# Kernel optimization log

Hardware: AMD Instinct MI355X
Metric: run time of the kernel (lower is better)

Reference implementation:

```python
import math
import jax, jax.numpy as jnp
import numpy as np

N, H, W = 512, 256, 256


def setup_inputs() -> dict:
    key = jax.random.key(0)
    k1, k2, k3 = jax.random.split(key, 3)
    # means uniform over the image plane, as in the torch __init__
    means = jax.random.uniform(k1, (N, 2), jnp.float32) * jnp.array([W, H], jnp.float32)
    # rgbs default 0.5 -> logit 0; perturb slightly for a non-degenerate test point
    rgb_logits = 0.1 * jax.random.normal(k2, (N, 3), jnp.float32)
    opacity_logits = jnp.zeros((N,), jnp.float32)
    # cholesky init: diag = log(expm1(scale)), off-diag 0 (scale = sqrt(H*W/N)*0.5)
    scale = math.sqrt(H * W / N) * 0.5
    diag = math.log(math.expm1(scale))
    cholesky_raw = jnp.stack([
        jnp.full((N,), diag, jnp.float32) + 0.05 * jax.random.normal(k3, (N,), jnp.float32),
        jnp.zeros((N,), jnp.float32),
        jnp.full((N,), diag, jnp.float32),
    ], axis=1)
    return {"means": means, "cholesky_raw": cholesky_raw,
            "rgb_logits": rgb_logits, "opacity_logits": opacity_logits}


def _render(means, cholesky_raw, rgb_logits, opacity_logits):
    # --- project_gaussians_cholesky: Cholesky -> covariance -> conic (inverse cov) ---
    L11 = jax.nn.softplus(cholesky_raw[:, 0])
    L21 = cholesky_raw[:, 1]
    L22 = jax.nn.softplus(cholesky_raw[:, 2])
    s00 = L11 * L11          # Sigma = L L^T
    s01 = L11 * L21
    s11 = L21 * L21 + L22 * L22
    det = (L11 * L22) ** 2   # det(Sigma)
    a = s11 / det            # conic = Sigma^{-1}, packed (a, b, c)
    b = -s01 / det
    c = s00 / det

    rgbs = jax.nn.sigmoid(rgb_logits)          # [N,3]
    opac = jax.nn.sigmoid(opacity_logits)      # [N]

    # --- rasterize: dense per-pixel evaluation, alpha-composited in gaussian order ---
    px = jnp.arange(W, dtype=jnp.float32) + 0.5
    py = jnp.arange(H, dtype=jnp.float32) + 0.5
    dX = means[:, 0, None, None] - px[None, None, :]   # [N,1,W]
    dY = means[:, 1, None, None] - py[None, :, None]   # [N,H,1]
    a3 = a[:, None, None]; b3 = b[:, None, None]; c3 = c[:, None, None]
    sigma = 0.5 * (a3 * dX * dX + c3 * dY * dY) + b3 * dX * dY   # [N,H,W]
    alpha = jnp.minimum(opac[:, None, None] * jnp.exp(-sigma), 0.999)

    # transmittance T_i = prod_{j<i} (1 - alpha_j), via exclusive cumsum in log space
    log1m = jnp.log1p(-alpha)
    logT = jnp.concatenate([jnp.zeros((1, H, W), alpha.dtype),
                            jnp.cumsum(log1m, axis=0)[:-1]], axis=0)
    vis = alpha * jnp.exp(logT)                # [N,H,W] compositing weight

    img = jnp.einsum('nhw,nc->hwc', vis, rgbs)     # [H,W,3]
    wsum = jnp.sum(vis, axis=0)                    # [H,W]

    # upscale gradients: d alpha / d(pixel x,y) per gaussian, composited with T
    gx = a3 * dX + b3 * dY
    gy = b3 * dX + c3 * dY
    dx_img = jnp.einsum('nhw,nc->hwc', vis * gx, rgbs)
    dy_img = jnp.einsum('nhw,nc->hwc', vis * gy, rgbs)
    dxy_img = jnp.einsum('nhw,nc->hwc', vis * (gx * gy - b3), rgbs)
    return img, wsum, dx_img, dy_img, dxy_img


def reference(means, cholesky_raw, rgb_logits, opacity_logits):
    img, wsum, dx_img, dy_img, dxy_img = _render(means, cholesky_raw, rgb_logits, opacity_logits)
    render = jnp.transpose(img, (2, 0, 1))  # CHW
    return (render, img, wsum, dx_img, dy_img, dxy_img)
```

## Files before the change

### kernel.cpp

```cpp
#include <hip/hip_runtime.h>
#include <math.h>

#define NG 512
#define HH 256
#define WW 256
#define TILE 8
#define TXN (WW / TILE)
#define TYN (HH / TILE)
#define NTILES (TXN * TYN)
#define CHUNKS 8
#define NACC 13
#define S_CUT 12.0f

__device__ __forceinline__ float softplus_f(float x) {
    if (x > 20.0f) return x;
    if (x < -20.0f) return expf(x);
    return log1pf(expf(x));
}

__device__ __forceinline__ float sigmoid_f(float x) {
    return 1.0f / (1.0f + expf(-x));
}

__global__ void prep_kernel(const float* __restrict__ means,
                            const float* __restrict__ chol,
                            const float* __restrict__ rgbl,
                            const float* __restrict__ opl,
                            float* __restrict__ params,
                            int4* __restrict__ tb) {
    int n = blockIdx.x * blockDim.x + threadIdx.x;
    if (n >= NG) return;
    float L11 = softplus_f(chol[3*n + 0]);
    float L21 = chol[3*n + 1];
    float L22 = softplus_f(chol[3*n + 2]);
    float s00 = L11 * L11;
    float s01 = L11 * L21;
    float s11 = L21 * L21 + L22 * L22;
    float d  = L11 * L22;
    float inv = 1.0f / (d * d);
    float mx = means[2*n + 0];
    float my = means[2*n + 1];
    float* p = params + 12 * n;
    p[0] = mx;
    p[1] = my;
    p[2] =  s11 * inv;
    p[3] = -s01 * inv;
    p[4] =  s00 * inv;
    p[5] = sigmoid_f(opl[n]);
    p[6] = sigmoid_f(rgbl[3*n + 0]);
    p[7] = sigmoid_f(rgbl[3*n + 1]);
    p[8] = sigmoid_f(rgbl[3*n + 2]);
    p[9] = 0.0f; p[10] = 0.0f; p[11] = 0.0f;

    float ex = sqrtf(2.0f * S_CUT * s00);
    float ey = sqrtf(2.0f * S_CUT * s11);
    int4 r;
    r.x = max(0,       (int)floorf((mx - ex) * (1.0f / TILE)));
    r.y = min(TXN - 1, (int)floorf((mx + ex) * (1.0f / TILE)));
    r.z = max(0,       (int)floorf((my - ey) * (1.0f / TILE)));
    r.w = min(TYN - 1, (int)floorf((my + ey) * (1.0f / TILE)));
    tb[n] = r;
}

__global__ __launch_bounds__(512, 8)
void render_kernel(const float* __restrict__ params,
                   const int4* __restrict__ tb,
                   float* __restrict__ out) {
    const int lane = threadIdx.x & 63;
    const int wv   = threadIdx.x >> 6;
    const int tx   = blockIdx.x & (TXN - 1);
    const int ty   = blockIdx.x >> 5;
    const int x0   = tx * TILE;
    const int y0   = ty * TILE;
    const float px = (float)(x0 + (lane & 7)) + 0.5f;
    const float py = (float)(y0 + (lane >> 3)) + 0.5f;

    int4 bb = tb[threadIdx.x];
    bool hit = (tx >= bb.x) && (tx <= bb.y) && (ty >= bb.z) && (ty <= bb.w);
    unsigned long long m = __ballot(hit ? 1 : 0);

    const float4* __restrict__ g4 = (const float4*)params;
    const int cbase = wv * 64;

    float T = 1.0f;
    float ir = 0.f, ig = 0.f, ib = 0.f, wsum = 0.f;
    float xr = 0.f, xg = 0.f, xb = 0.f;
    float yr = 0.f, yg = 0.f, yb = 0.f;
    float qr = 0.f, qg = 0.f, qb = 0.f;

    while (m) {
        int n = __builtin_ctzll(m);
        m &= (m - 1);
        int gi = __builtin_amdgcn_readfirstlane(cbase + n);
        float4 P0 = g4[3*gi + 0];
        float4 P1 = g4[3*gi + 1];
        float4 P2 = g4[3*gi + 2];
        float dX = P0.x - px;
        float dY = P0.y - py;
        float a = P0.z, b = P0.w, c = P1.x, opac = P1.y;
        float gx = a * dX + b * dY;
        float gy = b * dX + c * dY;
        float s  = 0.5f * (dX * gx + dY * gy);
        float e  = __expf(-s);
        float alpha = fminf(opac * e, 0.999f);
        float vis = alpha * T;
        T = T - alpha * T;
        wsum += vis;
        float r = P1.z, g = P1.w, bcol = P2.x;
        ir += vis * r;  ig += vis * g;  ib += vis * bcol;
        float vgx = vis * gx;
        float vgy = vis * gy;
        xr += vgx * r;  xg += vgx * g;  xb += vgx * bcol;
        yr += vgy * r;  yg += vgy * g;  yb += vgy * bcol;
        float q  = gx * gy - b;
        float vq = vis * q;
        qr += vq * r;   qg += vq * g;   qb += vq * bcol;
    }

    __shared__ float Tl[CHUNKS][64];
    __shared__ float accL[NACC][CHUNKS][64];
    Tl[wv][lane] = T;
    __syncthreads();

    float scale = 1.0f;
    for (int i = 0; i < wv; ++i) scale *= Tl[i][lane];

    accL[ 0][wv][lane] = ir   * scale;
    accL[ 1][wv][lane] = ig   * scale;
    accL[ 2][wv][lane] = ib   * scale;
    accL[ 3][wv][lane] = wsum * scale;
    accL[ 4][wv][lane] = xr   * scale;
    accL[ 5][wv][lane] = xg   * scale;
    accL[ 6][wv][lane] = xb   * scale;
    accL[ 7][wv][lane] = yr   * scale;
    accL[ 8][wv][lane] = yg   * scale;
    accL[ 9][wv][lane] = yb   * scale;
    accL[10][wv][lane] = qr   * scale;
    accL[11][wv][lane] = qg   * scale;
    accL[12][wv][lane] = qb   * scale;
    __syncthreads();

    const int HW = HH * WW;
    for (int v = threadIdx.x; v < 64 * NACC; v += 512) {
        int pp   = v / NACC;
        int comp = v - pp * NACC;
        float s = 0.f;
        #pragma unroll
        for (int cch = 0; cch < CHUNKS; ++cch) s += accL[comp][cch][pp];
        int p = (y0 + (pp >> 3)) * WW + x0 + (pp & 7);
        if (comp < 3) {
            out[comp * HW + p] = s;
            out[3 * HW + 3 * p + comp] = s;
        } else if (comp == 3) {
            out[6 * HW + p] = s;
        } else if (comp < 7) {
            out[7 * HW + 3 * p + (comp - 4)] = s;
        } else if (comp < 10) {
            out[10 * HW + 3 * p + (comp - 7)] = s;
        } else {
            out[13 * HW + 3 * p + (comp - 10)] = s;
        }
    }
}

extern "C" void kernel_launch(void* const* d_in, const int* in_sizes, int n_in,
                              void* d_out, int out_size, void* d_ws, size_t ws_size,
                              hipStream_t stream) {
    const float* means = (const float*)d_in[0];
    const float* chol  = (const float*)d_in[1];
    const float* rgbl  = (const float*)d_in[2];
    const float* opl   = (const float*)d_in[3];
    float* out = (float*)d_out;
    float* params = (float*)d_ws;
    int4*  tb     = (int4*)((char*)d_ws + 24 * 1024);

    prep_kernel<<<dim3(2), dim3(256), 0, stream>>>(means, chol, rgbl, opl, params, tb);
    render_kernel<<<dim3(NTILES), dim3(512), 0, stream>>>(params, tb, out);
}
```

Before: 71.73 us.

## Fuse gaussian preprocessing into render kernel with per-block LDS parameters

Removes the separate prep kernel and has every render block recompute all 512 gaussians' conic, colors, opacity and tile-overlap test itself, storing parameters in shared memory. The per-gaussian parameter reads then come from LDS instead of global memory, and one kernel launch plus the inter-kernel dependency disappear. In exchange every one of the 1024 blocks redoes the softplus, sigmoid and sqrt work for all gaussians. The LDS buffer is reused for the accumulator reduction. The bounding test now uses float comparisons against tile edges instead of integer tile indices.

```diff
diff --git a/kernel.cpp b/kernel.cpp
--- a/kernel.cpp
+++ b/kernel.cpp
@@ -22,52 +22,15 @@
     return 1.0f / (1.0f + expf(-x));
 }
 
-__global__ void prep_kernel(const float* __restrict__ means,
-                            const float* __restrict__ chol,
-                            const float* __restrict__ rgbl,
-                            const float* __restrict__ opl,
-                            float* __restrict__ params,
-                            int4* __restrict__ tb) {
-    int n = blockIdx.x * blockDim.x + threadIdx.x;
-    if (n >= NG) return;
-    float L11 = softplus_f(chol[3*n + 0]);
-    float L21 = chol[3*n + 1];
-    float L22 = softplus_f(chol[3*n + 2]);
-    float s00 = L11 * L11;
-    float s01 = L11 * L21;
-    float s11 = L21 * L21 + L22 * L22;
-    float d  = L11 * L22;
-    float inv = 1.0f / (d * d);
-    float mx = means[2*n + 0];
-    float my = means[2*n + 1];
-    float* p = params + 12 * n;
-    p[0] = mx;
-    p[1] = my;
-    p[2] =  s11 * inv;
-    p[3] = -s01 * inv;
-    p[4] =  s00 * inv;
-    p[5] = sigmoid_f(opl[n]);
-    p[6] = sigmoid_f(rgbl[3*n + 0]);
-    p[7] = sigmoid_f(rgbl[3*n + 1]);
-    p[8] = sigmoid_f(rgbl[3*n + 2]);
-    p[9] = 0.0f; p[10] = 0.0f; p[11] = 0.0f;
-
-    float ex = sqrtf(2.0f * S_CUT * s00);
-    float ey = sqrtf(2.0f * S_CUT * s11);
-    int4 r;
-    r.x = max(0,       (int)floorf((mx - ex) * (1.0f / TILE)));
-    r.y = min(TXN - 1, (int)floorf((mx + ex) * (1.0f / TILE)));
-    r.z = max(0,       (int)floorf((my - ey) * (1.0f / TILE)));
-    r.w = min(TYN - 1, (int)floorf((my + ey) * (1.0f / TILE)));
-    tb[n] = r;
-}
-
 __global__ __launch_bounds__(512, 8)
-void render_kernel(const float* __restrict__ params,
-                   const int4* __restrict__ tb,
+void render_kernel(const float* __restrict__ means,
+                   const float* __restrict__ chol,
+                   const float* __restrict__ rgbl,
+                   const float* __restrict__ opl,
                    float* __restrict__ out) {
-    const int lane = threadIdx.x & 63;
-    const int wv   = threadIdx.x >> 6;
+    const int tid  = threadIdx.x;
+    const int lane = tid & 63;
+    const int wv   = tid >> 6;
     const int tx   = blockIdx.x & (TXN - 1);
     const int ty   = blockIdx.x >> 5;
     const int x0   = tx * TILE;
@@ -75,11 +38,36 @@
     const float px = (float)(x0 + (lane & 7)) + 0.5f;
     const float py = (float)(y0 + (lane >> 3)) + 0.5f;
 
-    int4 bb = tb[threadIdx.x];
-    bool hit = (tx >= bb.x) && (tx <= bb.y) && (ty >= bb.z) && (ty <= bb.w);
+    __shared__ float shbuf[NACC * CHUNKS * 64];
+    __shared__ float Tl[CHUNKS][64];
+
+    bool hit;
+    {
+        float L11 = softplus_f(chol[3*tid + 0]);
+        float L21 = chol[3*tid + 1];
+        float L22 = softplus_f(chol[3*tid + 2]);
+        float s00 = L11 * L11;
+        float s01 = L11 * L21;
+        float s11 = L21 * L21 + L22 * L22;
+        float dd  = L11 * L22;
+        float inv = 1.0f / (dd * dd);
+        float mx  = means[2*tid + 0];
+        float my  = means[2*tid + 1];
+        float4* p4 = (float4*)shbuf;
+        p4[3*tid + 0] = make_float4(mx, my, s11 * inv, -s01 * inv);
+        p4[3*tid + 1] = make_float4(s00 * inv, sigmoid_f(opl[tid]),
+                                    sigmoid_f(rgbl[3*tid + 0]),
+                                    sigmoid_f(rgbl[3*tid + 1]));
+        p4[3*tid + 2] = make_float4(sigmoid_f(rgbl[3*tid + 2]), 0.f, 0.f, 0.f);
+        float ex = sqrtf(2.0f * S_CUT * s00);
+        float ey = sqrtf(2.0f * S_CUT * s11);
+        hit = (mx - ex < (float)(x0 + TILE)) && (mx + ex > (float)x0) &&
+              (my - ey < (float)(y0 + TILE)) && (my + ey > (float)y0);
+    }
     unsigned long long m = __ballot(hit ? 1 : 0);
+    __syncthreads();
 
-    const float4* __restrict__ g4 = (const float4*)params;
+    const float4* __restrict__ g4 = (const float4*)shbuf;
     const int cbase = wv * 64;
 
     float T = 1.0f;
@@ -117,36 +105,38 @@
         qr += vq * r;   qg += vq * g;   qb += vq * bcol;
     }
 
-    __shared__ float Tl[CHUNKS][64];
-    __shared__ float accL[NACC][CHUNKS][64];
     Tl[wv][lane] = T;
     __syncthreads();
 
     float scale = 1.0f;
     for (int i = 0; i < wv; ++i) scale *= Tl[i][lane];
 
-    accL[ 0][wv][lane] = ir   * scale;
-    accL[ 1][wv][lane] = ig   * scale;
-    accL[ 2][wv][lane] = ib   * scale;
-    accL[ 3][wv][lane] = wsum * scale;
-    accL[ 4][wv][lane] = xr   * scale;
-    accL[ 5][wv][lane] = xg   * scale;
-    accL[ 6][wv][lane] = xb   * scale;
-    accL[ 7][wv][lane] = yr   * scale;
-    accL[ 8][wv][lane] = yg   * scale;
-    accL[ 9][wv][lane] = yb   * scale;
-    accL[10][wv][lane] = qr   * scale;
-    accL[11][wv][lane] = qg   * scale;
-    accL[12][wv][lane] = qb   * scale;
+    float* accF = shbuf;
+    #define ACC(comp) accF[(comp) * (CHUNKS * 64) + wv * 64 + lane]
+    ACC(0)  = ir   * scale;
+    ACC(1)  = ig   * scale;
+    ACC(2)  = ib   * scale;
+    ACC(3)  = wsum * scale;
+    ACC(4)  = xr   * scale;
+    ACC(5)  = xg   * scale;
+    ACC(6)  = xb   * scale;
+    ACC(7)  = yr   * scale;
+    ACC(8)  = yg   * scale;
+    ACC(9)  = yb   * scale;
+    ACC(10) = qr   * scale;
+    ACC(11) = qg   * scale;
+    ACC(12) = qb   * scale;
+    #undef ACC
     __syncthreads();
 
     const int HW = HH * WW;
-    for (int v = threadIdx.x; v < 64 * NACC; v += 512) {
+    for (int v = tid; v < 64 * NACC; v += 512) {
         int pp   = v / NACC;
         int comp = v - pp * NACC;
         float s = 0.f;
         #pragma unroll
-        for (int cch = 0; cch < CHUNKS; ++cch) s += accL[comp][cch][pp];
+        for (int cch = 0; cch < CHUNKS; ++cch)
+            s += accF[comp * (CHUNKS * 64) + cch * 64 + pp];
         int p = (y0 + (pp >> 3)) * WW + x0 + (pp & 7);
         if (comp < 3) {
             out[comp * HW + p] = s;
@@ -171,9 +161,6 @@
     const float* rgbl  = (const float*)d_in[2];
     const float* opl   = (const float*)d_in[3];
     float* out = (float*)d_out;
-    float* params = (float*)d_ws;
-    int4*  tb     = (int4*)((char*)d_ws + 24 * 1024);
 
-    prep_kernel<<<dim3(2), dim3(256), 0, stream>>>(means, chol, rgbl, opl, params, tb);
-    render_kernel<<<dim3(NTILES), dim3(512), 0, stream>>>(params, tb, out);
+    render_kernel<<<dim3(NTILES), dim3(512), 0, stream>>>(means, chol, rgbl, opl, out);
 }
```

After: 74.19 us. 1.03x slower.
